# Performance work log

Measured on AMD Instinct MI355X. Metric: run time of the kernel, lower is better.

Reference implementation:

```python
import jax, jax.numpy as jnp
import numpy as np

B, S, E, H = 2, 2048, 1024, 16
D = E // H  # head_size = 64


def setup_inputs() -> dict:
    key = jax.random.key(0)
    ks = jax.random.split(key, 11)
    sc = 0.02
    return {
        "q": jax.random.normal(ks[0], (B, S, E), jnp.float32),
        "k": jax.random.normal(ks[1], (B, S, E), jnp.float32),
        "v": jax.random.normal(ks[2], (B, S, E), jnp.float32),
        "Wq": jax.random.normal(ks[3], (E, E), jnp.float32) * sc,
        "bq": jnp.zeros((E,), jnp.float32),
        "Wk": jax.random.normal(ks[4], (E, E), jnp.float32) * sc,
        "bk": jnp.zeros((E,), jnp.float32),
        "Wv": jax.random.normal(ks[5], (E, E), jnp.float32) * sc,
        "bv": jnp.zeros((E,), jnp.float32),
        "Wo": jax.random.normal(ks[6], (E, E), jnp.float32) * sc,
        "bo": jnp.zeros((E,), jnp.float32),
    }


def reference(q, k, v, Wq, bq, Wk, bk, Wv, bv, Wo, bo):
    # torch Linear: y = x @ W.T + b
    qh = (q @ Wq.T + bq).reshape(B, S, H, D)
    kh = (k @ Wk.T + bk).reshape(B, S, H, D)
    vh = (v @ Wv.T + bv).reshape(B, S, H, D)
    # NOTE: module scales by 1/sqrt(num_heads), not 1/sqrt(head_size)
    scores = jnp.einsum('bqhe,bkhe->bhqk', qh, kh) / jnp.sqrt(jnp.float32(H))
    attn = jax.nn.softmax(scores, axis=-1)  # dropout is identity in eval
    out = jnp.einsum('bhql,blhd->bqhd', attn, vh)  # [B,S,H,D]
    out = out.reshape(B, S, E)
    return out @ Wo.T + bo
```

## Files before the change

kernel.cpp:

```cpp
#include <hip/hip_runtime.h>

typedef __bf16 bf16x8 __attribute__((ext_vector_type(8)));
typedef __bf16 bf16x4 __attribute__((ext_vector_type(4)));
typedef float  f32x4  __attribute__((ext_vector_type(4)));
typedef short  s16x4  __attribute__((ext_vector_type(4)));

#define AS1 __attribute__((address_space(1)))
#define AS3 __attribute__((address_space(3)))

__device__ inline void gload_lds16(const void* g, void* l) {
  __builtin_amdgcn_global_load_lds((AS1 void*)(g), (AS3 void*)(l), 16, 0, 0);
}

#if __has_builtin(__builtin_amdgcn_exp2f)
#define EXP2(x) __builtin_amdgcn_exp2f(x)
#else
#define EXP2(x) exp2f(x)
#endif

#if __has_builtin(__builtin_amdgcn_mfma_f32_16x16x16bf16_1k)
#define PV_K16 1
#define MFMA16(a, b, c) __builtin_amdgcn_mfma_f32_16x16x16bf16_1k(a, b, c, 0, 0, 0)
#else
#define PV_K16 0
#endif

__device__ inline short bf2s(__bf16 x) {
  union { __bf16 b; short s; } u; u.b = x; return u.s;
}

#define CB 2
#define CS 2048
#define CE 1024
#define CH 16
#define CD 64
#define GM 4096
#define GN 1024
#define GK 1024

#define QSCALE 0.36067376022224087f

#define WS_WQ  0
#define WS_WK  1048576
#define WS_WV  2097152
#define WS_WO  3145728
#define WS_QH  16777216
#define WS_KH  20971520
#define WS_VT  25165824
#define WS_AO  4194304

__global__ __launch_bounds__(256) void convert_w(
    const float* __restrict__ wq, const float* __restrict__ wk,
    const float* __restrict__ wv, const float* __restrict__ wo,
    __bf16* __restrict__ ws) {
  long widx = ((long)blockIdx.x * 256 + threadIdx.x) * 8;
  int a = (int)(widx >> 20);
  long within = widx & 1048575;
  const float* src = (a == 0 ? wq : (a == 1 ? wk : (a == 2 ? wv : wo))) + within;
  __bf16* dst = ws + widx;
  float4 f0 = *(const float4*)src;
  float4 f1 = *(const float4*)(src + 4);
  bf16x8 o;
  o[0] = (__bf16)f0.x; o[1] = (__bf16)f0.y; o[2] = (__bf16)f0.z; o[3] = (__bf16)f0.w;
  o[4] = (__bf16)f1.x; o[5] = (__bf16)f1.y; o[6] = (__bf16)f1.z; o[7] = (__bf16)f1.w;
  *(bf16x8*)dst = o;
}

__global__ __launch_bounds__(256, 3) void qkv_gemm(
    const float* __restrict__ Aq, const float* __restrict__ Ak, const float* __restrict__ Av,
    const __bf16* __restrict__ Wq, const __bf16* __restrict__ Wk, const __bf16* __restrict__ Wv,
    const float* __restrict__ bq, const float* __restrict__ bk, const float* __restrict__ bv,
    __bf16* __restrict__ Qh, __bf16* __restrict__ Kh, __bf16* __restrict__ Vt) {
  const int mode = blockIdx.z;
  const float* A   = mode == 0 ? Aq : (mode == 1 ? Ak : Av);
  const __bf16* Bw = mode == 0 ? Wq : (mode == 1 ? Wk : Wv);
  const float* bias = mode == 0 ? bq : (mode == 1 ? bk : bv);

  __shared__ __bf16 As[8192];
  __shared__ __bf16 Bs[8192];
  const int tid = threadIdx.x;
  const int w = tid >> 6, l = tid & 63;
  const int wm = w >> 1, wn = w & 1;
  const int orig = blockIdx.y * gridDim.x + blockIdx.x;
  const int cpx = (gridDim.x * gridDim.y) >> 3;
  const int wgid = (orig & 7) * cpx + (orig >> 3);
  const int bm = (wgid / gridDim.x) * 128, bn = (wgid % gridDim.x) * 128;
  const int lr = l & 15, lq = l >> 4;
  f32x4 acc[4][4] = {};
  const int srow = w * 8 + (l >> 3);
  const int scol = ((l & 7) ^ ((l >> 3) & 7)) * 8;
  const float*  ga0 = A  + (size_t)(bm + srow) * GK + scol;
  const __bf16* gb0 = Bw + (size_t)(bn + srow) * GK + scol;
  const int dstg = w * 64 + l;

  float4 a0[4], a1[4];
  for (int i = 0; i < 4; i++) {
    const float* src = ga0 + (size_t)(i * 32) * GK;
    a0[i] = *(const float4*)src;
    a1[i] = *(const float4*)(src + 4);
  }

  for (int k0 = 0; k0 < GK; k0 += 64) {
    __syncthreads();
    for (int i = 0; i < 4; i++)
      gload_lds16(gb0 + (size_t)(i * 32) * GK + k0, &Bs[(i * 256 + dstg) * 8]);
    for (int i = 0; i < 4; i++) {
      bf16x8 o8;
      o8[0] = (__bf16)a0[i].x; o8[1] = (__bf16)a0[i].y;
      o8[2] = (__bf16)a0[i].z; o8[3] = (__bf16)a0[i].w;
      o8[4] = (__bf16)a1[i].x; o8[5] = (__bf16)a1[i].y;
      o8[6] = (__bf16)a1[i].z; o8[7] = (__bf16)a1[i].w;
      *(bf16x8*)&As[(i * 256 + dstg) * 8] = o8;
    }
    __syncthreads();
    if (k0 + 64 < GK) {
      for (int i = 0; i < 4; i++) {
        const float* src = ga0 + (size_t)(i * 32) * GK + k0 + 64;
        a0[i] = *(const float4*)src;
        a1[i] = *(const float4*)(src + 4);
      }
    }
    for (int kk = 0; kk < 2; kk++) {
      bf16x8 af[4], bfr[4];
      for (int mi = 0; mi < 4; mi++) {
        const int row = wm * 64 + mi * 16 + lr;
        af[mi] = *(const bf16x8*)&As[(row * 8 + ((kk * 4 + lq) ^ (row & 7))) * 8];
      }
      for (int ni = 0; ni < 4; ni++) {
        const int row = wn * 64 + ni * 16 + lr;
        bfr[ni] = *(const bf16x8*)&Bs[(row * 8 + ((kk * 4 + lq) ^ (row & 7))) * 8];
      }
      for (int mi = 0; mi < 4; mi++)
        for (int ni = 0; ni < 4; ni++)
          acc[mi][ni] = __builtin_amdgcn_mfma_f32_16x16x32_bf16(af[mi], bfr[ni],
                                                                acc[mi][ni], 0, 0, 0);
    }
  }

  const int row0 = bm + wm * 64;
  const int col0 = bn + wn * 64;
  for (int ni = 0; ni < 4; ni++) {
    const int col = col0 + ni * 16 + lr;
    const float bb = bias[col];
    for (int mi = 0; mi < 4; mi++) {
      const int row = row0 + mi * 16 + lq * 4;
      if (mode == 0) {
        for (int r = 0; r < 4; r++)
          Qh[(size_t)(row + r) * GN + col] = (__bf16)((acc[mi][ni][r] + bb) * QSCALE);
      } else if (mode == 1) {
        for (int r = 0; r < 4; r++)
          Kh[(size_t)(row + r) * GN + col] = (__bf16)(acc[mi][ni][r] + bb);
      } else {
        const int b = row >> 11, s = row & 2047;
        const int h = col >> 6, d = col & 63;
        bf16x4 pk;
        for (int r = 0; r < 4; r++) pk[r] = (__bf16)(acc[mi][ni][r] + bb);
        *(bf16x4*)&Vt[(size_t)((b * CH + h) * CD + d) * CS + s] = pk;
      }
    }
  }
}

__global__ __launch_bounds__(256) void gemm_wo(const __bf16* __restrict__ Ain,
                                               const __bf16* __restrict__ Bw,
                                               const float* __restrict__ bias,
                                               float* __restrict__ O) {
  __shared__ __bf16 As[4096];
  __shared__ __bf16 Bs[8192];
  const int tid = threadIdx.x;
  const int w = tid >> 6, l = tid & 63;
  const int orig = blockIdx.y * gridDim.x + blockIdx.x;
  const int cpx = (gridDim.x * gridDim.y) >> 3;
  const int wgid = (orig & 7) * cpx + (orig >> 3);
  const int bm = (wgid / gridDim.x) * 64, bn = (wgid % gridDim.x) * 128;
  const int lr = l & 15, lq = l >> 4;
  f32x4 acc[4][2] = {};
  const int srow = w * 8 + (l >> 3);
  const int scol = ((l & 7) ^ ((l >> 3) & 7)) * 8;
  const __bf16* ga0 = Ain + (size_t)(bm + srow) * GK + scol;
  const __bf16* gb0 = Bw + (size_t)(bn + srow) * GK + scol;
  const int dstg = w * 64 + l;
  for (int k0 = 0; k0 < GK; k0 += 64) {
    __syncthreads();
    for (int i = 0; i < 2; i++)
      gload_lds16(ga0 + (size_t)(i * 32) * GK + k0, &As[(i * 256 + dstg) * 8]);
    for (int i = 0; i < 4; i++)
      gload_lds16(gb0 + (size_t)(i * 32) * GK + k0, &Bs[(i * 256 + dstg) * 8]);
    __syncthreads();
    for (int kk = 0; kk < 2; kk++) {
      bf16x8 af[4], bfr[2];
      for (int mi = 0; mi < 4; mi++) {
        const int row = mi * 16 + lr;
        af[mi] = *(const bf16x8*)&As[(row * 8 + ((kk * 4 + lq) ^ (row & 7))) * 8];
      }
      for (int ni = 0; ni < 2; ni++) {
        const int row = w * 32 + ni * 16 + lr;
        bfr[ni] = *(const bf16x8*)&Bs[(row * 8 + ((kk * 4 + lq) ^ (row & 7))) * 8];
      }
      for (int mi = 0; mi < 4; mi++)
        for (int ni = 0; ni < 2; ni++)
          acc[mi][ni] = __builtin_amdgcn_mfma_f32_16x16x32_bf16(af[mi], bfr[ni],
                                                                acc[mi][ni], 0, 0, 0);
    }
  }

  for (int ni = 0; ni < 2; ni++) {
    const int col = bn + w * 32 + ni * 16 + lr;
    const float bb = bias[col];
    for (int mi = 0; mi < 4; mi++) {
      const int row = bm + mi * 16 + lq * 4;
      for (int r = 0; r < 4; r++)
        O[(size_t)(row + r) * GN + col] = acc[mi][ni][r] + bb;
    }
  }
}

__global__ __launch_bounds__(256, 2) void attn(const __bf16* __restrict__ Qh,
                                               const __bf16* __restrict__ Kh,
                                               const __bf16* __restrict__ Vt,
                                               __bf16* __restrict__ AO) {
  __shared__ __bf16 Ks[8192];
  __shared__ __bf16 Vs[8192];

  const int tid = threadIdx.x, w = tid >> 6, l = tid & 63;
  const int lr = l & 15, lq = l >> 4;
  const int bx = blockIdx.x;
  const int bh = (bx & 7) * 4 + (bx >> 3);
  const int b = bh >> 4, h = bh & 15;
  const int q0 = blockIdx.y * 128 + w * 32;

  bf16x8 qf[2][2];
  for (int mi = 0; mi < 2; mi++)
    for (int kk = 0; kk < 2; kk++)
      qf[mi][kk] = *(const bf16x8*)&Qh[((size_t)b * CS + q0 + mi * 16 + lr) * CE + h * CD + kk * 32 + lq * 8];

  f32x4 o[2][4] = {};
  float lsum[2] = {0.f, 0.f};
#if !PV_K16
  const bool hi_half = (lq & 1);
#endif

  for (int kt = 0; kt < CS / 128; kt++) {
    __syncthreads();
    for (int i = 0; i < 4; i++) {
      const int j = w * 2 + (i >> 1), hf = i & 1;
      const int key = (hf * 64 + l) ^ ((j & 3) * 2);
      gload_lds16(&Kh[((size_t)b * CS + kt * 128 + key) * CE + h * CD + j * 8],
                  &Ks[(j * 128 + hf * 64) * 8]);
    }
    for (int i = 0; i < 4; i++) {
      const int j2 = w * 4 + i;
      const int d = l ^ ((j2 & 1) * 4);
      gload_lds16(&Vt[((size_t)bh * CD + d) * CS + kt * 128 + j2 * 8],
                  &Vs[(j2 * 64) * 8]);
    }
    __syncthreads();

    f32x4 sa[2][8] = {};
    for (int kk = 0; kk < 2; kk++) {
      bf16x8 kf[8];
      for (int ni = 0; ni < 8; ni++)
        kf[ni] = *(const bf16x8*)&Ks[((kk * 4 + lq) * 128 + ((ni * 16 + lr) ^ (lq * 2))) * 8];
      for (int mi = 0; mi < 2; mi++)
        for (int ni = 0; ni < 8; ni++)
          sa[mi][ni] = __builtin_amdgcn_mfma_f32_16x16x32_bf16(kf[ni], qf[mi][kk], sa[mi][ni], 0, 0, 0);
    }

#if PV_K16
    for (int ni = 0; ni < 8; ni++) {
      s16x4 pa4[2];
      for (int mi = 0; mi < 2; mi++)
        for (int r = 0; r < 4; r++) {
          const float p = EXP2(sa[mi][ni][r]);
          lsum[mi] += p;
          pa4[mi][r] = bf2s((__bf16)p);
        }
      const int j2 = ni * 2 + (lq >> 1);
      const int base = j2 * 64;
      const int sw = (j2 & 1) * 4;
      for (int di = 0; di < 4; di++) {
        const int dslot = (di * 16 + lr) ^ sw;
        const s16x4 vb4 = *(const s16x4*)&Vs[(base + dslot) * 8 + (lq & 1) * 4];
        for (int mi = 0; mi < 2; mi++)
          o[mi][di] = MFMA16(pa4[mi], vb4, o[mi][di]);
      }
    }
#else
    for (int ni = 0; ni < 8; ni++) {
      bf16x8 pa[2];
      for (int mi = 0; mi < 2; mi++) {
        bf16x8 f;
        for (int r = 0; r < 4; r++) {
          const float p = EXP2(sa[mi][ni][r]);
          lsum[mi] += p;
          const __bf16 bv2 = (__bf16)p;
          f[r]     = hi_half ? (__bf16)0.f : bv2;
          f[4 + r] = hi_half ? bv2 : (__bf16)0.f;
        }
        pa[mi] = f;
      }
      for (int di = 0; di < 4; di++) {
        const bf16x8 vbf = *(const bf16x8*)&Vs[((ni * 2 + (lq >> 1)) * 64 + ((di * 16 + lr) ^ ((lq >> 1) * 4))) * 8];
        for (int mi = 0; mi < 2; mi++)
          o[mi][di] = __builtin_amdgcn_mfma_f32_16x16x32_bf16(pa[mi], vbf, o[mi][di], 0, 0, 0);
      }
    }
#endif
  }

  for (int mi = 0; mi < 2; mi++) {
    lsum[mi] += __shfl_xor(lsum[mi], 16, 64);
    lsum[mi] += __shfl_xor(lsum[mi], 32, 64);
  }

  for (int mi = 0; mi < 2; mi++) {
    f32x4 rv;
    for (int r = 0; r < 4; r++) rv[r] = 1.0f / __shfl(lsum[mi], lq * 4 + r, 64);
    for (int di = 0; di < 4; di++)
      for (int r = 0; r < 4; r++) {
        const size_t s = q0 + mi * 16 + lq * 4 + r;
        AO[((size_t)b * CS + s) * CE + h * CD + di * 16 + lr] = (__bf16)(o[mi][di][r] * rv[r]);
      }
  }
}

extern "C" void kernel_launch(void* const* d_in, const int* in_sizes, int n_in,
                              void* d_out, int out_size, void* d_ws, size_t ws_size,
                              hipStream_t stream) {
  (void)in_sizes; (void)n_in; (void)out_size; (void)ws_size;
  const float* q  = (const float*)d_in[0];
  const float* k  = (const float*)d_in[1];
  const float* v  = (const float*)d_in[2];
  const float* Wq = (const float*)d_in[3];
  const float* bq = (const float*)d_in[4];
  const float* Wk = (const float*)d_in[5];
  const float* bk = (const float*)d_in[6];
  const float* Wv = (const float*)d_in[7];
  const float* bv = (const float*)d_in[8];
  const float* Wo = (const float*)d_in[9];
  const float* bo = (const float*)d_in[10];

  __bf16* ws = (__bf16*)d_ws;
  __bf16 *Wq_b = ws + WS_WQ, *Wk_b = ws + WS_WK, *Wv_b = ws + WS_WV, *Wo_b = ws + WS_WO;
  __bf16 *Qh = ws + WS_QH, *Kh = ws + WS_KH, *Vt = ws + WS_VT;
  __bf16 *AO = ws + WS_AO;

  convert_w<<<2048, 256, 0, stream>>>(Wq, Wk, Wv, Wo, ws);

  qkv_gemm<<<dim3(GN / 128, GM / 128, 3), 256, 0, stream>>>(
      q, k, v, Wq_b, Wk_b, Wv_b, bq, bk, bv, Qh, Kh, Vt);

  attn<<<dim3(CB * CH, CS / 128), 256, 0, stream>>>(Qh, Kh, Vt, AO);

  gemm_wo<<<dim3(GN / 128, GM / 64), 256, 0, stream>>>(AO, Wo_b, bo, (float*)d_out);
}
```

Baseline: 215.4 us.

## Fuse fp32-to-bf16 weight conversion into the QKV and output GEMMs

Removes the separate convert_w kernel and has the QKV and Wo GEMMs load fp32 weights directly, converting them to bf16 in registers before the LDS store. This drops one kernel launch and the extra write/read of 8 MB of bf16 weights. In exchange each GEMM tile reads twice the weight bytes from global memory, repeatedly across the M tiles. The async global_load_lds path for B is replaced with register loads, with a register prefetch in gemm_wo, which raises register pressure.

New measurement: 228.9 us. 6.3% more time.

```diff
diff --git a/kernel.cpp b/kernel.cpp
--- a/kernel.cpp
+++ b/kernel.cpp
@@ -27,6 +27,13 @@
 
 __device__ inline short bf2s(__bf16 x) {
   union { __bf16 b; short s; } u; u.b = x; return u.s;
+}
+
+__device__ inline bf16x8 cvt_f32x8_bf16(const float4& a, const float4& b) {
+  bf16x8 o;
+  o[0] = (__bf16)a.x; o[1] = (__bf16)a.y; o[2] = (__bf16)a.z; o[3] = (__bf16)a.w;
+  o[4] = (__bf16)b.x; o[5] = (__bf16)b.y; o[6] = (__bf16)b.z; o[7] = (__bf16)b.w;
+  return o;
 }
 
 #define CB 2
@@ -40,40 +47,19 @@
 
 #define QSCALE 0.36067376022224087f
 
-#define WS_WQ  0
-#define WS_WK  1048576
-#define WS_WV  2097152
-#define WS_WO  3145728
 #define WS_QH  16777216
 #define WS_KH  20971520
 #define WS_VT  25165824
 #define WS_AO  4194304
 
-__global__ __launch_bounds__(256) void convert_w(
-    const float* __restrict__ wq, const float* __restrict__ wk,
-    const float* __restrict__ wv, const float* __restrict__ wo,
-    __bf16* __restrict__ ws) {
-  long widx = ((long)blockIdx.x * 256 + threadIdx.x) * 8;
-  int a = (int)(widx >> 20);
-  long within = widx & 1048575;
-  const float* src = (a == 0 ? wq : (a == 1 ? wk : (a == 2 ? wv : wo))) + within;
-  __bf16* dst = ws + widx;
-  float4 f0 = *(const float4*)src;
-  float4 f1 = *(const float4*)(src + 4);
-  bf16x8 o;
-  o[0] = (__bf16)f0.x; o[1] = (__bf16)f0.y; o[2] = (__bf16)f0.z; o[3] = (__bf16)f0.w;
-  o[4] = (__bf16)f1.x; o[5] = (__bf16)f1.y; o[6] = (__bf16)f1.z; o[7] = (__bf16)f1.w;
-  *(bf16x8*)dst = o;
-}
-
 __global__ __launch_bounds__(256, 3) void qkv_gemm(
     const float* __restrict__ Aq, const float* __restrict__ Ak, const float* __restrict__ Av,
-    const __bf16* __restrict__ Wq, const __bf16* __restrict__ Wk, const __bf16* __restrict__ Wv,
+    const float* __restrict__ Wq, const float* __restrict__ Wk, const float* __restrict__ Wv,
     const float* __restrict__ bq, const float* __restrict__ bk, const float* __restrict__ bv,
     __bf16* __restrict__ Qh, __bf16* __restrict__ Kh, __bf16* __restrict__ Vt) {
   const int mode = blockIdx.z;
-  const float* A   = mode == 0 ? Aq : (mode == 1 ? Ak : Av);
-  const __bf16* Bw = mode == 0 ? Wq : (mode == 1 ? Wk : Wv);
+  const float* A  = mode == 0 ? Aq : (mode == 1 ? Ak : Av);
+  const float* Bw = mode == 0 ? Wq : (mode == 1 ? Wk : Wv);
   const float* bias = mode == 0 ? bq : (mode == 1 ? bk : bv);
 
   __shared__ __bf16 As[8192];
@@ -89,8 +75,8 @@
   f32x4 acc[4][4] = {};
   const int srow = w * 8 + (l >> 3);
   const int scol = ((l & 7) ^ ((l >> 3) & 7)) * 8;
-  const float*  ga0 = A  + (size_t)(bm + srow) * GK + scol;
-  const __bf16* gb0 = Bw + (size_t)(bn + srow) * GK + scol;
+  const float* ga0 = A  + (size_t)(bm + srow) * GK + scol;
+  const float* gb0 = Bw + (size_t)(bn + srow) * GK + scol;
   const int dstg = w * 64 + l;
 
   float4 a0[4], a1[4];
@@ -102,16 +88,16 @@
 
   for (int k0 = 0; k0 < GK; k0 += 64) {
     __syncthreads();
+    float4 b0[4], b1[4];
+    for (int i = 0; i < 4; i++) {
+      const float* src = gb0 + (size_t)(i * 32) * GK + k0;
+      b0[i] = *(const float4*)src;
+      b1[i] = *(const float4*)(src + 4);
+    }
     for (int i = 0; i < 4; i++)
-      gload_lds16(gb0 + (size_t)(i * 32) * GK + k0, &Bs[(i * 256 + dstg) * 8]);
-    for (int i = 0; i < 4; i++) {
-      bf16x8 o8;
-      o8[0] = (__bf16)a0[i].x; o8[1] = (__bf16)a0[i].y;
-      o8[2] = (__bf16)a0[i].z; o8[3] = (__bf16)a0[i].w;
-      o8[4] = (__bf16)a1[i].x; o8[5] = (__bf16)a1[i].y;
-      o8[6] = (__bf16)a1[i].z; o8[7] = (__bf16)a1[i].w;
-      *(bf16x8*)&As[(i * 256 + dstg) * 8] = o8;
-    }
+      *(bf16x8*)&As[(i * 256 + dstg) * 8] = cvt_f32x8_bf16(a0[i], a1[i]);
+    for (int i = 0; i < 4; i++)
+      *(bf16x8*)&Bs[(i * 256 + dstg) * 8] = cvt_f32x8_bf16(b0[i], b1[i]);
     __syncthreads();
     if (k0 + 64 < GK) {
       for (int i = 0; i < 4; i++) {
@@ -162,7 +148,7 @@
 }
 
 __global__ __launch_bounds__(256) void gemm_wo(const __bf16* __restrict__ Ain,
-                                               const __bf16* __restrict__ Bw,
+                                               const float* __restrict__ Bw,
                                                const float* __restrict__ bias,
                                                float* __restrict__ O) {
   __shared__ __bf16 As[4096];
@@ -178,15 +164,30 @@
   const int srow = w * 8 + (l >> 3);
   const int scol = ((l & 7) ^ ((l >> 3) & 7)) * 8;
   const __bf16* ga0 = Ain + (size_t)(bm + srow) * GK + scol;
-  const __bf16* gb0 = Bw + (size_t)(bn + srow) * GK + scol;
+  const float*  gb0 = Bw  + (size_t)(bn + srow) * GK + scol;
   const int dstg = w * 64 + l;
+
+  float4 b0[4], b1[4];
+  for (int i = 0; i < 4; i++) {
+    const float* src = gb0 + (size_t)(i * 32) * GK;
+    b0[i] = *(const float4*)src;
+    b1[i] = *(const float4*)(src + 4);
+  }
+
   for (int k0 = 0; k0 < GK; k0 += 64) {
     __syncthreads();
     for (int i = 0; i < 2; i++)
       gload_lds16(ga0 + (size_t)(i * 32) * GK + k0, &As[(i * 256 + dstg) * 8]);
     for (int i = 0; i < 4; i++)
-      gload_lds16(gb0 + (size_t)(i * 32) * GK + k0, &Bs[(i * 256 + dstg) * 8]);
-    __syncthreads();
+      *(bf16x8*)&Bs[(i * 256 + dstg) * 8] = cvt_f32x8_bf16(b0[i], b1[i]);
+    __syncthreads();
+    if (k0 + 64 < GK) {
+      for (int i = 0; i < 4; i++) {
+        const float* src = gb0 + (size_t)(i * 32) * GK + k0 + 64;
+        b0[i] = *(const float4*)src;
+        b1[i] = *(const float4*)(src + 4);
+      }
+    }
     for (int kk = 0; kk < 2; kk++) {
       bf16x8 af[4], bfr[2];
       for (int mi = 0; mi < 4; mi++) {
@@ -341,16 +342,13 @@
   const float* bo = (const float*)d_in[10];
 
   __bf16* ws = (__bf16*)d_ws;
-  __bf16 *Wq_b = ws + WS_WQ, *Wk_b = ws + WS_WK, *Wv_b = ws + WS_WV, *Wo_b = ws + WS_WO;
   __bf16 *Qh = ws + WS_QH, *Kh = ws + WS_KH, *Vt = ws + WS_VT;
   __bf16 *AO = ws + WS_AO;
 
-  convert_w<<<2048, 256, 0, stream>>>(Wq, Wk, Wv, Wo, ws);
-
   qkv_gemm<<<dim3(GN / 128, GM / 128, 3), 256, 0, stream>>>(
-      q, k, v, Wq_b, Wk_b, Wv_b, bq, bk, bv, Qh, Kh, Vt);
+      q, k, v, Wq, Wk, Wv, bq, bk, bv, Qh, Kh, Vt);
 
   attn<<<dim3(CB * CH, CS / 128), 256, 0, stream>>>(Qh, Kh, Vt, AO);
 
-  gemm_wo<<<dim3(GN / 128, GM / 64), 256, 0, stream>>>(AO, Wo_b, bo, (float*)d_out);
-}
+  gemm_wo<<<dim3(GN / 128, GM / 64), 256, 0, stream>>>(AO, Wo, bo, (float*)d_out);
+}
```
